# Performance work log

Hardware: AMD Instinct MI355X
Metric: run time of the kernel (lower is better)

Reference implementation:

```python
import jax, jax.numpy as jnp
import numpy as np

U, S, D, ORDER, R, B = 339, 5825, 128, 3, 32, 500000
N = U + S
NNZ = 200000
H = D // 2  # MLP hidden = dimension // 2 = 64
EPS = 1e-5


def _xavier(key, shape):
    lim = (6.0 / (shape[0] + shape[1])) ** 0.5
    return jax.random.uniform(key, shape, minval=-lim, maxval=lim, dtype=jnp.float32)


def setup_inputs() -> dict:
    key = jax.random.key(0)
    ks = jax.random.split(key, 16)
    # --- sparse bipartite adjacency (binary, symmetrized, sym-normalized) ---
    rng = np.random.default_rng(0)
    flat = rng.choice(U * S, size=NNZ, replace=False)
    u = (flat // S).astype(np.int64)
    s = (flat % S).astype(np.int64) + U
    rows = np.concatenate([u, s])
    cols = np.concatenate([s, u])
    deg = np.bincount(rows, minlength=N).astype(np.float32)
    dinv = np.where(deg > 0, deg ** -0.5, 0.0).astype(np.float32)
    vals = dinv[rows] * dinv[cols]
    inp = {
        'uEmbeds': _xavier(ks[0], (U, D)),
        'iEmbeds': _xavier(ks[1], (S, D)),
        'uHyper': _xavier(ks[2], (R, D)),
        'iHyper': _xavier(ks[3], (R, D)),
        'W1': _xavier(ks[4], (2 * D, H)), 'b1': jnp.zeros((H,), jnp.float32),
        'g1': jnp.ones((H,), jnp.float32), 'be1': jnp.zeros((H,), jnp.float32),
        'W2': _xavier(ks[5], (H, H)), 'b2': jnp.zeros((H,), jnp.float32),
        'g2': jnp.ones((H,), jnp.float32), 'be2': jnp.zeros((H,), jnp.float32),
        'W3': _xavier(ks[6], (H, 1)), 'b3': jnp.zeros((1,), jnp.float32),
        'adj_vals': jnp.asarray(vals),
        'adj_rows': jnp.asarray(rows, dtype=jnp.int32),
        'adj_cols': jnp.asarray(cols, dtype=jnp.int32),
        'userIdx': jax.random.randint(ks[7], (B,), 0, U, dtype=jnp.int32),
        'servIdx': jax.random.randint(ks[8], (B,), 0, S, dtype=jnp.int32),
    }
    return inp


def _layernorm(x, g, b):
    mu = jnp.mean(x, axis=-1, keepdims=True)
    var = jnp.var(x, axis=-1, keepdims=True)
    return (x - mu) * jax.lax.rsqrt(var + EPS) * g + b


def reference(uEmbeds, iEmbeds, uHyper, iHyper,
              W1, b1, g1, be1, W2, b2, g2, be2, W3, b3,
              adj_vals, adj_rows, adj_cols, userIdx, servIdx):
    # multi-order GCN propagation via sparse COO spmm
    embeds = jnp.concatenate([uEmbeds, iEmbeds], axis=0)  # [N, D]
    for _ in range(ORDER):
        embeds = jax.ops.segment_sum(adj_vals[:, None] * embeds[adj_cols],
                                     adj_rows, num_segments=N)
    # hypergraph projection (embeds are detached in the original)
    e = jax.lax.stop_gradient(embeds)
    hyperU = e[:U] @ (uHyper.T @ uHyper)   # [U, D]
    hyperI = e[U:] @ (iHyper.T @ iHyper)   # [S, D]
    x = jnp.concatenate([hyperU[userIdx], hyperI[servIdx]], axis=1)  # [B, 2D]
    h = jax.nn.relu(_layernorm(x @ W1 + b1, g1, be1))
    h = jax.nn.relu(_layernorm(h @ W2 + b2, g2, be2))
    return h @ W3 + b3  # [B, 1]
```

## Files before the change

kernel.cpp:

```cpp
#include <hip/hip_runtime.h>
#include <hip/hip_bf16.h>

#define U_CNT 339
#define S_CNT 5825
#define N_CNT 6164
#define D_DIM 128
#define R_DIM 32
#define B_CNT 500000
#define NNZ_U 200000
#define H_DIM 64
#define LN_EPS 1e-5f

#define SPAD 5856
#define UPAD 352
#define KT_S 183
#define KT_U 11
#define NT_S 365
#define NT_U 22
#define U_KCHUNK 23

#define ET_U16 (D_DIM * SPAD)
#define PKS_U16 (KT_U * NT_S * 512)
#define PKU_U16 (KT_S * NT_U * 512)
#define WT_U16  (H_DIM * UPAD)

#define PRE_S_UNITS 183
#define PRE_U_UNITS 11
#define PRE_UT_END (PRE_S_UNITS + PRE_U_UNITS)
#define PRE_EDGE_UNITS ((NNZ_U + 255) / 256)
#define PRE_UNITS (PRE_UT_END + PRE_EDGE_UNITS)

#define HV_GU_END 484
#define HV_YT_END 660
#define HV_BLOCKS 669

#define WF_B1   4096
#define WF_G1   4160
#define WF_BE1  4224
#define WF_B2   4288
#define WF_G2   4352
#define WF_BE2  4416
#define WF_W3   4480
#define WF_B3   4544
#define WF_TOT  4545

#define MLP_BLOCKS 1024

typedef __hip_bfloat16 bf16;
typedef __attribute__((ext_vector_type(8))) short sh8;
typedef __attribute__((ext_vector_type(4))) float f4v;

__device__ __forceinline__ float b2f(bf16 x) { return __bfloat162float(x); }
__device__ __forceinline__ unsigned short f2bs(float f) {
    union { bf16 b; unsigned short s; } u;
    u.b = __float2bfloat16(f);
    return u.s;
}
__device__ __forceinline__ float bu2f(unsigned int lo16) {
    return __uint_as_float(lo16 << 16);
}
__device__ __forceinline__ float ldf(const void* p, long i, int isf32) {
    return isf32 ? ((const float*)p)[i] : b2f(((const bf16*)p)[i]);
}
__device__ __forceinline__ int detect_f32(const void* uE) {
    const unsigned short* p = (const unsigned short*)uE;
    int lane = threadIdx.x & 63;
    unsigned short v = p[2 * lane];
    int e = (v >> 7) & 0xFF;
    unsigned long long m = __ballot(e >= 127);
    return (m != 0ull) ? 1 : 0;
}

template<int CTRL>
__device__ __forceinline__ float dpp_add(float x) {
    int t = __builtin_amdgcn_update_dpp(0, __float_as_int(x), CTRL, 0xF, 0xF, false);
    return x + __int_as_float(t);
}
__device__ __forceinline__ float rowsum16(float x) {
    x = dpp_add<0xB1>(x);
    x = dpp_add<0x4E>(x);
    x = dpp_add<0x124>(x);
    x = dpp_add<0x128>(x);
    return x;
}

__global__ void __launch_bounds__(256)
k_pre(const void* __restrict__ iE,
      unsigned short* __restrict__ EtHi, unsigned short* __restrict__ EtLo,
      const int* __restrict__ rows, const int* __restrict__ cols,
      const void* __restrict__ vals,
      unsigned short* __restrict__ PkS, unsigned short* __restrict__ PkU,
      float* __restrict__ uEt,
      const void* __restrict__ uE) {
    __shared__ float ls[32 * 129];
    int tid = threadIdx.x;
    int isf32 = detect_f32(uE);
    int unit = blockIdx.x;
    if (unit < PRE_S_UNITS) {
        int sg0 = unit * 32;
        int nl = tid >> 3, dbase = (tid & 7) * 16;
        int s = sg0 + nl;
        #pragma unroll
        for (int i = 0; i < 16; ++i) {
            int d = dbase + i;
            float v = (s < S_CNT) ? ldf(iE, (long)s * D_DIM + d, isf32) : 0.f;
            ls[nl * 129 + d] = v;
        }
        __syncthreads();
        int nl2 = tid & 31;
        int s2 = sg0 + nl2;
        #pragma unroll
        for (int i = 0; i < 16; ++i) {
            int d = (tid >> 5) * 16 + i;
            float v = ls[nl2 * 129 + d];
            unsigned short hi = f2bs(v);
            unsigned short lo = f2bs(v - bu2f(hi));
            EtHi[(size_t)d * SPAD + s2] = hi;
            EtLo[(size_t)d * SPAD + s2] = lo;
        }
    } else if (unit < PRE_UT_END) {
        int ug0 = (unit - PRE_S_UNITS) * 32;
        int nl = tid >> 3, dbase = (tid & 7) * 16;
        int u = ug0 + nl;
        #pragma unroll
        for (int i = 0; i < 16; ++i) {
            int d = dbase + i;
            float v = (u < U_CNT) ? ldf(uE, (long)u * D_DIM + d, isf32) : 0.f;
            ls[nl * 129 + d] = v;
        }
        __syncthreads();
        int nl2 = tid & 31;
        int u2 = ug0 + nl2;
        if (u2 < U_CNT) {
            #pragma unroll
            for (int i = 0; i < 16; ++i) {
                int d = (tid >> 5) * 16 + i;
                uEt[(size_t)d * UPAD + u2] = ls[nl2 * 129 + d];
            }
        }
    } else {
        int e = (unit - PRE_UT_END) * 256 + tid;
        if (e < NNZ_U) {
            int r = rows[e];
            if (r < U_CNT) {
                int u = r, s = cols[e] - U_CNT;
                unsigned short w = f2bs(ldf(vals, e, isf32));
                int kt = u >> 5, kq = (u >> 3) & 3, j = u & 7;
                int nt = s >> 4, nn = s & 15;
                PkS[((kt * NT_S + nt) * 64 + kq * 16 + nn) * 8 + j] = w;
                int kt2 = s >> 5, kq2 = (s >> 3) & 3, j2 = s & 7;
                int nt2 = u >> 4, nn2 = u & 15;
                PkU[((kt2 * NT_U + nt2) * 64 + kq2 * 16 + nn2) * 8 + j2] = w;
            }
        }
    }
}

__global__ void __launch_bounds__(512)
k_heavy(const unsigned short* __restrict__ EtHi, const unsigned short* __restrict__ EtLo,
        const unsigned short* __restrict__ PkU,
        float* __restrict__ Gu, float* __restrict__ yT,
        const void* __restrict__ uHy, const void* __restrict__ iHy,
        const void* __restrict__ W1, const void* __restrict__ W2,
        const void* __restrict__ b1, const void* __restrict__ g1,
        const void* __restrict__ be1, const void* __restrict__ b2,
        const void* __restrict__ g2, const void* __restrict__ be2,
        const void* __restrict__ W3, const void* __restrict__ b3,
        float* __restrict__ Pc, float* __restrict__ Wf,
        unsigned short* __restrict__ Wb,
        const void* __restrict__ uE) {
    __shared__ __align__(16) float sm[6688];
    int tid = threadIdx.x;
    int bid = blockIdx.x;
    if (bid < HV_YT_END) {
        int wv = tid >> 6, lane = tid & 63;
        int am = lane & 15, aq = lane >> 4;
        const sh8* Bp = (const sh8*)PkU;
        float4* red = (float4*)sm;
        int k0 = wv * U_KCHUNK, k1 = min(KT_S, k0 + U_KCHUNK);
        f4v acc = {0.f, 0.f, 0.f, 0.f};
        int mt, nt;
        if (bid < HV_GU_END) {
            mt = bid / NT_U; nt = bid % NT_U;
            for (int kt = k0; kt < k1; ++kt) {
                sh8 aa = Bp[(kt * NT_U + mt) * 64 + lane];
                sh8 bb = Bp[(kt * NT_U + nt) * 64 + lane];
                acc = __builtin_amdgcn_mfma_f32_16x16x32_bf16(aa, bb, acc, 0, 0, 0);
            }
        } else {
            int tile = bid - HV_GU_END;
            mt = tile / NT_U; nt = tile % NT_U;
            const unsigned short* rH = EtHi + (size_t)(mt * 16 + am) * SPAD;
            const unsigned short* rL = EtLo + (size_t)(mt * 16 + am) * SPAD;
            for (int kt = k0; kt < k1; ++kt) {
                sh8 bb = Bp[(kt * NT_U + nt) * 64 + lane];
                sh8 ah = *(const sh8*)(rH + kt * 32 + aq * 8);
                sh8 al = *(const sh8*)(rL + kt * 32 + aq * 8);
                acc = __builtin_amdgcn_mfma_f32_16x16x32_bf16(ah, bb, acc, 0, 0, 0);
                acc = __builtin_amdgcn_mfma_f32_16x16x32_bf16(al, bb, acc, 0, 0, 0);
            }
        }
        red[wv * 64 + lane] = make_float4(acc[0], acc[1], acc[2], acc[3]);
        __syncthreads();
        if (wv == 0) {
            float4 v = red[lane];
            #pragma unroll
            for (int w2 = 1; w2 < 8; ++w2) {
                float4 p = red[w2 * 64 + lane];
                v.x += p.x; v.y += p.y; v.z += p.z; v.w += p.w;
            }
            float vr[4] = {v.x, v.y, v.z, v.w};
            float* dst = (bid < HV_GU_END) ? Gu : yT;
            #pragma unroll
            for (int reg = 0; reg < 4; ++reg)
                dst[(size_t)(mt * 16 + aq * 4 + reg) * UPAD + nt * 16 + am] = vr[reg];
        }
        return;
    }
    int rb = bid - HV_YT_END;
    int isf32 = detect_f32(uE);
    if (rb == 8) {
        for (int i = tid; i < 4096; i += 512) {
            int j = i & 7, lane = (i >> 3) & 63, kh = (i >> 9) & 1, t = i >> 10;
            int k = kh * 32 + ((lane >> 4) & 3) * 8 + j;
            int n = t * 16 + (lane & 15);
            Wb[i] = f2bs(ldf(W2, k * 64 + n, isf32));
        }
        for (int i = tid; i < WF_TOT - 4096; i += 512) {
            int g = 4096 + i;
            float v;
            if      (g < WF_G1)  v = ldf(b1,  g - WF_B1,   isf32);
            else if (g < WF_BE1) v = ldf(g1,  g - WF_G1,   isf32);
            else if (g < WF_B2)  v = ldf(be1, g - WF_BE1,  isf32);
            else if (g < WF_G2)  v = ldf(b2,  g - WF_B2,   isf32);
            else if (g < WF_BE2) v = ldf(g2,  g - WF_G2,   isf32);
            else if (g < WF_W3)  v = ldf(be2, g - WF_BE2,  isf32);
            else if (g < WF_B3)  v = ldf(W3,  g - WF_W3,   isf32);
            else                 v = ldf(b3,  0,           isf32);
            Wf[g] = v;
        }
        return;
    }
    int side = rb >> 2;
    int j0 = (rb & 3) * 16;
    const void* Hy = side ? iHy : uHy;
    long wbase = (long)side * D_DIM * H_DIM;
    float* Hs = sm;
    float* Ws = sm + R_DIM * 129;
    float* Ts = Ws + D_DIM * 16;
    if (isf32) {
        const float* H = (const float*)Hy;
        for (int i = tid; i < R_DIM * D_DIM; i += 512)
            Hs[(i >> 7) * 129 + (i & 127)] = H[i];
        const float* Wp = (const float*)W1 + wbase;
        for (int i = tid; i < D_DIM * 16; i += 512)
            Ws[i] = Wp[(i >> 4) * H_DIM + j0 + (i & 15)];
    } else {
        const unsigned short* H = (const unsigned short*)Hy;
        for (int i = tid; i < R_DIM * D_DIM; i += 512)
            Hs[(i >> 7) * 129 + (i & 127)] = bu2f(H[i]);
        const unsigned short* Wp = (const unsigned short*)W1 + wbase;
        for (int i = tid; i < D_DIM * 16; i += 512)
            Ws[i] = bu2f(Wp[(i >> 4) * H_DIM + j0 + (i & 15)]);
    }
    __syncthreads();
    for (int idx = tid; idx < R_DIM * 16; idx += 512) {
        int a = idx >> 4, j = idx & 15;
        float acc = 0.f;
        #pragma unroll 8
        for (int d = 0; d < D_DIM; ++d)
            acc = fmaf(Hs[a * 129 + d], Ws[d * 16 + j], acc);
        Ts[idx] = acc;
    }
    __syncthreads();
    for (int idx = tid; idx < D_DIM * 16; idx += 512) {
        int d = idx >> 4, j = idx & 15;
        float acc = 0.f;
        #pragma unroll
        for (int a = 0; a < R_DIM; ++a)
            acc = fmaf(Hs[a * 129 + d], Ts[a * 16 + j], acc);
        Pc[side * D_DIM * H_DIM + d * H_DIM + j0 + j] = acc;
    }
}

__global__ void __launch_bounds__(256)
k_mid(const float* __restrict__ uEt, const float* __restrict__ Gu,
      const float* __restrict__ yT, const float* __restrict__ Pc,
      const float* __restrict__ Wf,
      unsigned short* __restrict__ wTH, unsigned short* __restrict__ wTL,
      float* __restrict__ A) {
    __shared__ float gr[UPAD];
    __shared__ float te[2 * D_DIM], ty[2 * D_DIM];
    int r = blockIdx.x, tid = threadIdx.x;
    for (int i = tid; i < U_CNT; i += 256) gr[i] = Gu[(size_t)r * UPAD + i];
    __syncthreads();
    {
        int d = tid & 127, h = tid >> 7;
        int a0 = h ? 170 : 0, a1 = h ? U_CNT : 170;
        float se = 0.f, sy = 0.f;
        const float* erow = uEt + (size_t)d * UPAD;
        const float* yrow = yT + (size_t)d * UPAD;
        #pragma unroll 4
        for (int a = a0; a < a1; ++a) {
            float g = gr[a];
            se = fmaf(g, erow[a], se);
            sy = fmaf(g, yrow[a], sy);
        }
        te[h * 128 + d] = se; ty[h * 128 + d] = sy;
    }
    __syncthreads();
    if (tid < 128) { te[tid] += te[128 + tid]; ty[tid] += ty[128 + tid]; }
    __syncthreads();
    int j = tid & 63;
    if (tid < 64) {
        float w = 0.f;
        #pragma unroll 8
        for (int d = 0; d < D_DIM; ++d)
            w = fmaf(te[d], Pc[D_DIM * H_DIM + d * H_DIM + j], w);
        unsigned short hi = f2bs(w);
        unsigned short lo = f2bs(w - bu2f(hi));
        wTH[(size_t)j * UPAD + r] = hi;
        wTL[(size_t)j * UPAD + r] = lo;
    } else if (tid < 128) {
        float au = Wf[WF_B1 + j];
        #pragma unroll 8
        for (int d = 0; d < D_DIM; ++d)
            au = fmaf(ty[d], Pc[d * H_DIM + j], au);
        A[(size_t)r * H_DIM + j] = au;
    }
}

__global__ void __launch_bounds__(256)
k_as(const unsigned short* __restrict__ wTH, const unsigned short* __restrict__ wTL,
     const unsigned short* __restrict__ PkS, float* __restrict__ A) {
    __shared__ float ls[16][65];
    int nt = blockIdx.x;
    int tid = threadIdx.x, wv = tid >> 6, lane = tid & 63;
    int am = lane & 15, aq = lane >> 4;
    const sh8* Bp = (const sh8*)PkS;
    const unsigned short* rH = wTH + (size_t)(wv * 16 + am) * UPAD;
    const unsigned short* rL = wTL + (size_t)(wv * 16 + am) * UPAD;
    f4v acc0 = {0.f, 0.f, 0.f, 0.f}, acc1 = acc0;
    #pragma unroll
    for (int kt = 0; kt < KT_U; ++kt) {
        sh8 bb = Bp[(kt * NT_S + nt) * 64 + lane];
        sh8 ah = *(const sh8*)(rH + kt * 32 + aq * 8);
        sh8 al = *(const sh8*)(rL + kt * 32 + aq * 8);
        acc0 = __builtin_amdgcn_mfma_f32_16x16x32_bf16(ah, bb, acc0, 0, 0, 0);
        acc1 = __builtin_amdgcn_mfma_f32_16x16x32_bf16(al, bb, acc1, 0, 0, 0);
    }
    #pragma unroll
    for (int reg = 0; reg < 4; ++reg)
        ls[am][wv * 16 + aq * 4 + reg] = acc0[reg] + acc1[reg];
    __syncthreads();
    int sl = tid >> 4, j0 = (tid & 15) * 4;
    int s = nt * 16 + sl;
    if (s < S_CNT) {
        float4 v = make_float4(ls[sl][j0], ls[sl][j0 + 1], ls[sl][j0 + 2], ls[sl][j0 + 3]);
        *(float4*)(A + (size_t)(U_CNT + s) * H_DIM + j0) = v;
    }
}

__global__ void __launch_bounds__(256)
HyperModel_65755949301857_kernel(
      const float* __restrict__ A, const int* __restrict__ userIdx,
      const int* __restrict__ servIdx, const float* __restrict__ Wf,
      const unsigned short* __restrict__ Wb,
      void* __restrict__ out, const void* __restrict__ uE) {
    int tid = threadIdx.x;
    int wv = tid >> 6, lane = tid & 63;
    int isf32 = detect_f32(uE);
    int m = lane & 15, quad = lane >> 4;

    const sh8* Bp = (const sh8*)Wb;
    sh8 b00 = Bp[0 * 64 + lane], b01 = Bp[1 * 64 + lane];
    sh8 b10 = Bp[2 * 64 + lane], b11 = Bp[3 * 64 + lane];
    sh8 b20 = Bp[4 * 64 + lane], b21 = Bp[5 * 64 + lane];
    sh8 b30 = Bp[6 * 64 + lane], b31 = Bp[7 * 64 + lane];
    float b2c0 = Wf[WF_B2 + m],      b2c1 = Wf[WF_B2 + 16 + m];
    float b2c2 = Wf[WF_B2 + 32 + m], b2c3 = Wf[WF_B2 + 48 + m];
    float g2c0 = Wf[WF_G2 + m],      g2c1 = Wf[WF_G2 + 16 + m];
    float g2c2 = Wf[WF_G2 + 32 + m], g2c3 = Wf[WF_G2 + 48 + m];
    float e2c0 = Wf[WF_BE2 + m],      e2c1 = Wf[WF_BE2 + 16 + m];
    float e2c2 = Wf[WF_BE2 + 32 + m], e2c3 = Wf[WF_BE2 + 48 + m];
    float w3c0 = Wf[WF_W3 + m],      w3c1 = Wf[WF_W3 + 16 + m];
    float w3c2 = Wf[WF_W3 + 32 + m], w3c3 = Wf[WF_W3 + 48 + m];
    float b3v = Wf[WF_B3];
    const float* G1l = Wf + WF_G1 + quad * 8;
    const float* BE1l = Wf + WF_BE1 + quad * 8;

    const long TILES = B_CNT / 16;
    const long stride = (long)gridDim.x * 4;
    long tile = (long)blockIdx.x * 4 + wv;
    if (tile >= TILES) return;

    int r0 = (int)(tile * 16 + m);
    const float4* Au = (const float4*)(A + (long)userIdx[r0] * 64);
    const float4* As = (const float4*)(A + (long)(servIdx[r0] + U_CNT) * 64);
    float4 bu0 = Au[quad * 2], bu1 = Au[quad * 2 + 1], bu2 = Au[8 + quad * 2], bu3 = Au[9 + quad * 2];
    float4 bs0 = As[quad * 2], bs1 = As[quad * 2 + 1], bs2 = As[8 + quad * 2], bs3 = As[9 + quad * 2];
    long tn = tile + stride;
    int uin = 0, sin = 0;
    if (tn < TILES) {
        int rn = (int)(tn * 16 + m);
        uin = userIdx[rn];
        sin = servIdx[rn] + U_CNT;
    }

    while (true) {
        float zl[8], zh[8];
        zl[0] = bu0.x + bs0.x; zl[1] = bu0.y + bs0.y; zl[2] = bu0.z + bs0.z; zl[3] = bu0.w + bs0.w;
        zl[4] = bu1.x + bs1.x; zl[5] = bu1.y + bs1.y; zl[6] = bu1.z + bs1.z; zl[7] = bu1.w + bs1.w;
        zh[0] = bu2.x + bs2.x; zh[1] = bu2.y + bs2.y; zh[2] = bu2.z + bs2.z; zh[3] = bu2.w + bs2.w;
        zh[4] = bu3.x + bs3.x; zh[5] = bu3.y + bs3.y; zh[6] = bu3.z + bs3.z; zh[7] = bu3.w + bs3.w;

        long tcur = tile;
        bool have_next = (tn < TILES);
        if (have_next) {
            const float4* Au2 = (const float4*)(A + (long)uin * 64);
            const float4* As2 = (const float4*)(A + (long)sin * 64);
            bu0 = Au2[quad * 2]; bu1 = Au2[quad * 2 + 1]; bu2 = Au2[8 + quad * 2]; bu3 = Au2[9 + quad * 2];
            bs0 = As2[quad * 2]; bs1 = As2[quad * 2 + 1]; bs2 = As2[8 + quad * 2]; bs3 = As2[9 + quad * 2];
            long tnn = tn + stride;
            if (tnn < TILES) {
                int rnn = (int)(tnn * 16 + m);
                uin = userIdx[rnn];
                sin = servIdx[rnn] + U_CNT;
            }
            tile = tn;
            tn = tnn;
        }

        float s = 0.f, q = 0.f;
        #pragma unroll
        for (int j = 0; j < 8; ++j) {
            s += zl[j] + zh[j];
            q = fmaf(zl[j], zl[j], q);
            q = fmaf(zh[j], zh[j], q);
        }
        s += __shfl_xor(s, 16, 64); s += __shfl_xor(s, 32, 64);
        q += __shfl_xor(q, 16, 64); q += __shfl_xor(q, 32, 64);
        float mu = s * (1.f / 64.f);
        float rs = rsqrtf(q * (1.f / 64.f) - mu * mu + LN_EPS);
        float nm = -mu * rs;

        sh8 a0, a1;
        #pragma unroll
        for (int j = 0; j < 8; ++j) {
            float h0 = fmaxf(fmaf(fmaf(zl[j], rs, nm), G1l[j],      BE1l[j]),      0.f);
            float h1 = fmaxf(fmaf(fmaf(zh[j], rs, nm), G1l[32 + j], BE1l[32 + j]), 0.f);
            a0[j] = (short)f2bs(h0);
            a1[j] = (short)f2bs(h1);
        }

        f4v acc0 = {0.f, 0.f, 0.f, 0.f}, acc1 = acc0, acc2 = acc0, acc3 = acc0;
        acc0 = __builtin_amdgcn_mfma_f32_16x16x32_bf16(a0, b00, acc0, 0, 0, 0);
        acc0 = __builtin_amdgcn_mfma_f32_16x16x32_bf16(a1, b01, acc0, 0, 0, 0);
        acc1 = __builtin_amdgcn_mfma_f32_16x16x32_bf16(a0, b10, acc1, 0, 0, 0);
        acc1 = __builtin_amdgcn_mfma_f32_16x16x32_bf16(a1, b11, acc1, 0, 0, 0);
        acc2 = __builtin_amdgcn_mfma_f32_16x16x32_bf16(a0, b20, acc2, 0, 0, 0);
        acc2 = __builtin_amdgcn_mfma_f32_16x16x32_bf16(a1, b21, acc2, 0, 0, 0);
        acc3 = __builtin_amdgcn_mfma_f32_16x16x32_bf16(a0, b30, acc3, 0, 0, 0);
        acc3 = __builtin_amdgcn_mfma_f32_16x16x32_bf16(a1, b31, acc3, 0, 0, 0);

        float y0[4], y1[4], y2[4], y3[4];
        float srow[4], qrow[4];
        #pragma unroll
        for (int reg = 0; reg < 4; ++reg) {
            y0[reg] = acc0[reg] + b2c0;
            y1[reg] = acc1[reg] + b2c1;
            y2[reg] = acc2[reg] + b2c2;
            y3[reg] = acc3[reg] + b2c3;
            srow[reg] = (y0[reg] + y1[reg]) + (y2[reg] + y3[reg]);
            float qa = y0[reg] * y0[reg];
            qa = fmaf(y1[reg], y1[reg], qa);
            qa = fmaf(y2[reg], y2[reg], qa);
            qa = fmaf(y3[reg], y3[reg], qa);
            qrow[reg] = qa;
        }
        #pragma unroll
        for (int reg = 0; reg < 4; ++reg) {
            srow[reg] = rowsum16(srow[reg]);
            qrow[reg] = rowsum16(qrow[reg]);
        }
        float o[4];
        #pragma unroll
        for (int reg = 0; reg < 4; ++reg) {
            float mu2 = srow[reg] * (1.f / 64.f);
            float rs2 = rsqrtf(qrow[reg] * (1.f / 64.f) - mu2 * mu2 + LN_EPS);
            float nm2 = -mu2 * rs2;
            float t0 = fmaxf(fmaf(fmaf(y0[reg], rs2, nm2), g2c0, e2c0), 0.f);
            float t1 = fmaxf(fmaf(fmaf(y1[reg], rs2, nm2), g2c1, e2c1), 0.f);
            float t2 = fmaxf(fmaf(fmaf(y2[reg], rs2, nm2), g2c2, e2c2), 0.f);
            float t3 = fmaxf(fmaf(fmaf(y3[reg], rs2, nm2), g2c3, e2c3), 0.f);
            o[reg] = fmaf(t0, w3c0, fmaf(t1, w3c1, fmaf(t2, w3c2, t3 * w3c3)));
        }
        #pragma unroll
        for (int reg = 0; reg < 4; ++reg) o[reg] = rowsum16(o[reg]);
        if (m == 0) {
            long rb = tcur * 16 + quad * 4;
            if (isf32) {
                float4 v = make_float4(o[0] + b3v, o[1] + b3v, o[2] + b3v, o[3] + b3v);
                *(float4*)((float*)out + rb) = v;
            } else {
                ushort4 v;
                v.x = f2bs(o[0] + b3v);
                v.y = f2bs(o[1] + b3v);
                v.z = f2bs(o[2] + b3v);
                v.w = f2bs(o[3] + b3v);
                *(ushort4*)((bf16*)out + rb) = v;
            }
        }
        if (!have_next) break;
    }
}

extern "C" __attribute__((visibility("default")))
void kernel_launch(void* const* d_in, const int* in_sizes, int n_in,
                   void* d_out, int out_size, void* d_ws, size_t ws_size,
                   hipStream_t stream) {
    const void* uE   = d_in[0];
    const void* iE   = d_in[1];
    const void* uHy  = d_in[2];
    const void* iHy  = d_in[3];
    const void* W1   = d_in[4];
    const void* b1   = d_in[5];
    const void* g1   = d_in[6];
    const void* be1  = d_in[7];
    const void* W2   = d_in[8];
    const void* b2   = d_in[9];
    const void* g2   = d_in[10];
    const void* be2  = d_in[11];
    const void* W3   = d_in[12];
    const void* b3   = d_in[13];
    const void* adj_vals = d_in[14];
    const int*  adj_rows = (const int*)d_in[15];
    const int*  adj_cols = (const int*)d_in[16];
    const int*  userIdx  = (const int*)d_in[17];
    const int*  servIdx  = (const int*)d_in[18];

    char* w = (char*)d_ws;
    size_t off = 0;
    auto alloc = [&](size_t bytes) -> char* {
        char* p = w + off;
        off += (bytes + 255) & ~(size_t)255;
        return p;
    };
    unsigned short* EtHi = (unsigned short*)alloc((size_t)ET_U16 * 2);
    unsigned short* EtLo = (unsigned short*)alloc((size_t)ET_U16 * 2);
    float* Gu   = (float*)alloc((size_t)UPAD * UPAD * 4);
    float* yT   = (float*)alloc((size_t)D_DIM * UPAD * 4);
    float* uEt  = (float*)alloc((size_t)D_DIM * UPAD * 4);
    float* Pc   = (float*)alloc((size_t)2 * D_DIM * H_DIM * 4);
    float* A    = (float*)alloc((size_t)N_CNT * H_DIM * 4);
    float* Wf   = (float*)alloc((size_t)WF_TOT * 4);
    unsigned short* Wb = (unsigned short*)alloc((size_t)4096 * 2);
    unsigned short* PkS = (unsigned short*)alloc((size_t)PKS_U16 * 2);
    unsigned short* PkU = (unsigned short*)alloc((size_t)PKU_U16 * 2);
    unsigned short* wTH = (unsigned short*)alloc((size_t)WT_U16 * 2);
    unsigned short* wTL = (unsigned short*)alloc((size_t)WT_U16 * 2);
    size_t zspan = (size_t)((char*)(wTL + WT_U16) - (char*)PkS);

    hipMemsetAsync(PkS, 0, zspan, stream);
    k_pre<<<PRE_UNITS, 256, 0, stream>>>(iE, EtHi, EtLo, adj_rows, adj_cols,
                                         adj_vals, PkS, PkU, uEt, uE);
    k_heavy<<<HV_BLOCKS, 512, 0, stream>>>(EtHi, EtLo, PkU, Gu, yT,
                                           uHy, iHy, W1, W2, b1, g1, be1,
                                           b2, g2, be2, W3, b3,
                                           Pc, Wf, Wb, uE);
    k_mid<<<U_CNT, 256, 0, stream>>>(uEt, Gu, yT, Pc, Wf, wTH, wTL, A);
    k_as<<<NT_S, 256, 0, stream>>>(wTH, wTL, PkS, A);
    HyperModel_65755949301857_kernel<<<MLP_BLOCKS, 256, 0, stream>>>(
        A, userIdx, servIdx, Wf, Wb, d_out, uE);
}
```

Baseline: 210.8 us.

## Reassociate mid-stage products and run Gu-by-V on split-bf16 MFMA

The per-user mid kernel computed Gu·uEt and Gu·yT as fp32 dot products and then projected them through Pc. The new code reassociates this: it first forms V = [yT|uEt]ᵀ·Pc, a small 352x128 matrix packed in MFMA layout, then runs one Gu·V product on bf16 hi/lo split MFMAs across 44 blocks. Gu is now stored as hi/lo bf16 instead of fp32, and the wT buffers are no longer zeroed by the memset. This trades one extra launch and some precision (the lo·lo term is dropped) for far fewer scalar FMAs on the mid stage.

```diff
diff --git a/kernel.cpp b/kernel.cpp
--- a/kernel.cpp
+++ b/kernel.cpp
@@ -23,6 +23,8 @@
 #define PKS_U16 (KT_U * NT_S * 512)
 #define PKU_U16 (KT_S * NT_U * 512)
 #define WT_U16  (H_DIM * UPAD)
+#define GU_U16  (UPAD * UPAD)
+#define V_U16   (KT_U * 8 * 512)
 
 #define PRE_S_UNITS 183
 #define PRE_U_UNITS 11
@@ -131,12 +133,10 @@
         __syncthreads();
         int nl2 = tid & 31;
         int u2 = ug0 + nl2;
-        if (u2 < U_CNT) {
-            #pragma unroll
-            for (int i = 0; i < 16; ++i) {
-                int d = (tid >> 5) * 16 + i;
-                uEt[(size_t)d * UPAD + u2] = ls[nl2 * 129 + d];
-            }
+        #pragma unroll
+        for (int i = 0; i < 16; ++i) {
+            int d = (tid >> 5) * 16 + i;
+            uEt[(size_t)d * UPAD + u2] = (u2 < UPAD) ? ls[nl2 * 129 + d] : 0.f;
         }
     } else {
         int e = (unit - PRE_UT_END) * 256 + tid;
@@ -159,7 +159,8 @@
 __global__ void __launch_bounds__(512)
 k_heavy(const unsigned short* __restrict__ EtHi, const unsigned short* __restrict__ EtLo,
         const unsigned short* __restrict__ PkU,
-        float* __restrict__ Gu, float* __restrict__ yT,
+        unsigned short* __restrict__ GuHi, unsigned short* __restrict__ GuLo,
+        float* __restrict__ yT,
         const void* __restrict__ uHy, const void* __restrict__ iHy,
         const void* __restrict__ W1, const void* __restrict__ W2,
         const void* __restrict__ b1, const void* __restrict__ g1,
@@ -210,10 +211,19 @@
                 v.x += p.x; v.y += p.y; v.z += p.z; v.w += p.w;
             }
             float vr[4] = {v.x, v.y, v.z, v.w};
-            float* dst = (bid < HV_GU_END) ? Gu : yT;
-            #pragma unroll
-            for (int reg = 0; reg < 4; ++reg)
-                dst[(size_t)(mt * 16 + aq * 4 + reg) * UPAD + nt * 16 + am] = vr[reg];
+            if (bid < HV_GU_END) {
+                #pragma unroll
+                for (int reg = 0; reg < 4; ++reg) {
+                    size_t idx = (size_t)(mt * 16 + aq * 4 + reg) * UPAD + nt * 16 + am;
+                    unsigned short hi = f2bs(vr[reg]);
+                    GuHi[idx] = hi;
+                    GuLo[idx] = f2bs(vr[reg] - bu2f(hi));
+                }
+            } else {
+                #pragma unroll
+                for (int reg = 0; reg < 4; ++reg)
+                    yT[(size_t)(mt * 16 + aq * 4 + reg) * UPAD + nt * 16 + am] = vr[reg];
+            }
         }
         return;
     }
@@ -284,49 +294,74 @@
 }
 
 __global__ void __launch_bounds__(256)
-k_mid(const float* __restrict__ uEt, const float* __restrict__ Gu,
-      const float* __restrict__ yT, const float* __restrict__ Pc,
-      const float* __restrict__ Wf,
-      unsigned short* __restrict__ wTH, unsigned short* __restrict__ wTL,
-      float* __restrict__ A) {
-    __shared__ float gr[UPAD];
-    __shared__ float te[2 * D_DIM], ty[2 * D_DIM];
-    int r = blockIdx.x, tid = threadIdx.x;
-    for (int i = tid; i < U_CNT; i += 256) gr[i] = Gu[(size_t)r * UPAD + i];
-    __syncthreads();
-    {
-        int d = tid & 127, h = tid >> 7;
-        int a0 = h ? 170 : 0, a1 = h ? U_CNT : 170;
-        float se = 0.f, sy = 0.f;
-        const float* erow = uEt + (size_t)d * UPAD;
-        const float* yrow = yT + (size_t)d * UPAD;
-        #pragma unroll 4
-        for (int a = a0; a < a1; ++a) {
-            float g = gr[a];
-            se = fmaf(g, erow[a], se);
-            sy = fmaf(g, yrow[a], sy);
-        }
-        te[h * 128 + d] = se; ty[h * 128 + d] = sy;
-    }
-    __syncthreads();
-    if (tid < 128) { te[tid] += te[128 + tid]; ty[tid] += ty[128 + tid]; }
-    __syncthreads();
-    int j = tid & 63;
-    if (tid < 64) {
-        float w = 0.f;
-        #pragma unroll 8
-        for (int d = 0; d < D_DIM; ++d)
-            w = fmaf(te[d], Pc[D_DIM * H_DIM + d * H_DIM + j], w);
-        unsigned short hi = f2bs(w);
-        unsigned short lo = f2bs(w - bu2f(hi));
-        wTH[(size_t)j * UPAD + r] = hi;
-        wTL[(size_t)j * UPAD + r] = lo;
-    } else if (tid < 128) {
-        float au = Wf[WF_B1 + j];
-        #pragma unroll 8
-        for (int d = 0; d < D_DIM; ++d)
-            au = fmaf(ty[d], Pc[d * H_DIM + j], au);
-        A[(size_t)r * H_DIM + j] = au;
+k_midA(const float* __restrict__ yT, const float* __restrict__ uEt,
+       const float* __restrict__ Pc,
+       unsigned short* __restrict__ VHi, unsigned short* __restrict__ VLo) {
+    int bid = blockIdx.x;
+    int kt = bid >> 4, jg = bid & 15;
+    int tid = threadIdx.x;
+    int kl = tid & 31, jl = tid >> 5;
+    int k = kt * 32 + kl;
+    int j = jg * 8 + jl;
+    const float* S = (j < H_DIM) ? yT : uEt;
+    const float* P = Pc + ((j < H_DIM) ? (size_t)j
+                                       : (size_t)(D_DIM * H_DIM + j - H_DIM));
+    float acc = 0.f;
+    #pragma unroll 8
+    for (int d = 0; d < D_DIM; ++d)
+        acc = fmaf(S[(size_t)d * UPAD + k], P[(size_t)d * H_DIM], acc);
+    unsigned short hi = f2bs(acc);
+    unsigned short lo = f2bs(acc - bu2f(hi));
+    int kq = (k >> 3) & 3, jj = k & 7;
+    int nt = j >> 4, nn = j & 15;
+    size_t idx = ((size_t)(kt * 8 + nt) * 64 + kq * 16 + nn) * 8 + jj;
+    VHi[idx] = hi;
+    VLo[idx] = lo;
+}
+
+__global__ void __launch_bounds__(256)
+k_midB(const unsigned short* __restrict__ GuHi, const unsigned short* __restrict__ GuLo,
+       const unsigned short* __restrict__ VHi, const unsigned short* __restrict__ VLo,
+       const float* __restrict__ Wf, float* __restrict__ A,
+       unsigned short* __restrict__ wTH, unsigned short* __restrict__ wTL) {
+    int tid = threadIdx.x, wv = tid >> 6, lane = tid & 63;
+    int am = lane & 15, aq = lane >> 4;
+    int tile = blockIdx.x * 4 + wv;
+    int mt = tile >> 3, nt = tile & 7;
+    const sh8* BH = (const sh8*)VHi;
+    const sh8* BL = (const sh8*)VLo;
+    const unsigned short* rH = GuHi + (size_t)(mt * 16 + am) * UPAD;
+    const unsigned short* rL = GuLo + (size_t)(mt * 16 + am) * UPAD;
+    f4v acc = {0.f, 0.f, 0.f, 0.f};
+    #pragma unroll
+    for (int kt = 0; kt < KT_U; ++kt) {
+        sh8 bh = BH[(kt * 8 + nt) * 64 + lane];
+        sh8 bl = BL[(kt * 8 + nt) * 64 + lane];
+        sh8 ah = *(const sh8*)(rH + kt * 32 + aq * 8);
+        sh8 al = *(const sh8*)(rL + kt * 32 + aq * 8);
+        acc = __builtin_amdgcn_mfma_f32_16x16x32_bf16(ah, bh, acc, 0, 0, 0);
+        acc = __builtin_amdgcn_mfma_f32_16x16x32_bf16(ah, bl, acc, 0, 0, 0);
+        acc = __builtin_amdgcn_mfma_f32_16x16x32_bf16(al, bh, acc, 0, 0, 0);
+    }
+    if (nt < 4) {
+        int j = nt * 16 + am;
+        float b1j = Wf[WF_B1 + j];
+        #pragma unroll
+        for (int reg = 0; reg < 4; ++reg) {
+            int r = mt * 16 + aq * 4 + reg;
+            if (r < U_CNT) A[(size_t)r * H_DIM + j] = acc[reg] + b1j;
+        }
+    } else {
+        int j = nt * 16 + am - 64;
+        int r0 = mt * 16 + aq * 4;
+        ushort4 vh, vl;
+        unsigned short h;
+        h = f2bs(acc[0]); vh.x = h; vl.x = f2bs(acc[0] - bu2f(h));
+        h = f2bs(acc[1]); vh.y = h; vl.y = f2bs(acc[1] - bu2f(h));
+        h = f2bs(acc[2]); vh.z = h; vl.z = f2bs(acc[2] - bu2f(h));
+        h = f2bs(acc[3]); vh.w = h; vl.w = f2bs(acc[3] - bu2f(h));
+        *(ushort4*)(wTH + (size_t)j * UPAD + r0) = vh;
+        *(ushort4*)(wTL + (size_t)j * UPAD + r0) = vl;
     }
 }
 
@@ -548,7 +583,12 @@
     };
     unsigned short* EtHi = (unsigned short*)alloc((size_t)ET_U16 * 2);
     unsigned short* EtLo = (unsigned short*)alloc((size_t)ET_U16 * 2);
-    float* Gu   = (float*)alloc((size_t)UPAD * UPAD * 4);
+    unsigned short* GuHi = (unsigned short*)alloc((size_t)GU_U16 * 2);
+    unsigned short* GuLo = (unsigned short*)alloc((size_t)GU_U16 * 2);
+    unsigned short* VHi  = (unsigned short*)alloc((size_t)V_U16 * 2);
+    unsigned short* VLo  = (unsigned short*)alloc((size_t)V_U16 * 2);
+    unsigned short* wTH  = (unsigned short*)alloc((size_t)WT_U16 * 2);
+    unsigned short* wTL  = (unsigned short*)alloc((size_t)WT_U16 * 2);
     float* yT   = (float*)alloc((size_t)D_DIM * UPAD * 4);
     float* uEt  = (float*)alloc((size_t)D_DIM * UPAD * 4);
     float* Pc   = (float*)alloc((size_t)2 * D_DIM * H_DIM * 4);
@@ -557,18 +597,17 @@
     unsigned short* Wb = (unsigned short*)alloc((size_t)4096 * 2);
     unsigned short* PkS = (unsigned short*)alloc((size_t)PKS_U16 * 2);
     unsigned short* PkU = (unsigned short*)alloc((size_t)PKU_U16 * 2);
-    unsigned short* wTH = (unsigned short*)alloc((size_t)WT_U16 * 2);
-    unsigned short* wTL = (unsigned short*)alloc((size_t)WT_U16 * 2);
-    size_t zspan = (size_t)((char*)(wTL + WT_U16) - (char*)PkS);
+    size_t zspan = (size_t)((char*)(PkU + PKU_U16) - (char*)PkS);
 
     hipMemsetAsync(PkS, 0, zspan, stream);
     k_pre<<<PRE_UNITS, 256, 0, stream>>>(iE, EtHi, EtLo, adj_rows, adj_cols,
                                          adj_vals, PkS, PkU, uEt, uE);
-    k_heavy<<<HV_BLOCKS, 512, 0, stream>>>(EtHi, EtLo, PkU, Gu, yT,
+    k_heavy<<<HV_BLOCKS, 512, 0, stream>>>(EtHi, EtLo, PkU, GuHi, GuLo, yT,
                                            uHy, iHy, W1, W2, b1, g1, be1,
                                            b2, g2, be2, W3, b3,
                                            Pc, Wf, Wb, uE);
-    k_mid<<<U_CNT, 256, 0, stream>>>(uEt, Gu, yT, Pc, Wf, wTH, wTL, A);
+    k_midA<<<176, 256, 0, stream>>>(yT, uEt, Pc, VHi, VLo);
+    k_midB<<<44, 256, 0, stream>>>(GuHi, GuLo, VHi, VLo, Wf, A, wTH, wTL);
     k_as<<<NT_S, 256, 0, stream>>>(wTH, wTL, PkS, A);
     HyperModel_65755949301857_kernel<<<MLP_BLOCKS, 256, 0, stream>>>(
         A, userIdx, servIdx, Wf, Wb, d_out, uE);
```

Result: faster. 181.2 us (-14.0%).
